# Optimization experiments

Hardware: AMD Instinct MI355X
Metric: run time of the kernel (lower is better)

Reference implementation:

```python
import jax, jax.numpy as jnp
import numpy as np

EPS = 1e-5  # BatchNorm2d default eps
PAD = 7     # width padding; conv-transpose equiv pad = k-1-p = 15-1-7 = 7


def _conv(x, w):
    # NCHW conv, kernel (O,I,1,T), stride 1, padding (0, PAD)
    return jax.lax.conv_general_dilated(
        x, w, window_strides=(1, 1), padding=((0, 0), (PAD, PAD)),
        dimension_numbers=('NCHW', 'OIHW', 'NCHW'))


def setup_inputs() -> dict:
    key = jax.random.key(0)
    ks = jax.random.split(key, 4)
    B, H, D = 32, 64, 256          # batch, electrodes, time (= patch_size = codebook dim)
    C, K, T = 16, 2048, 15         # channel_size, codebook size, temp_kernel
    x = jax.random.normal(ks[0], (B, 1, H, D), dtype=jnp.float32)
    # xavier_uniform_ for both convs (fan_in/fan_out from torch conv weight shapes)
    lim_e = float(np.sqrt(6.0 / (1 * T + C * T)))
    w_enc = jax.random.uniform(ks[1], (C, 1, 1, T), jnp.float32, -lim_e, lim_e)
    lim_d = float(np.sqrt(6.0 / (C * T + 1 * T)))
    # torch ConvTranspose2d weight layout: (in_ch=C, out_ch=1, 1, T)
    w_dec = jax.random.uniform(ks[2], (C, 1, 1, T), jnp.float32, -lim_d, lim_d)
    gamma = jnp.ones((C,), jnp.float32)   # BatchNorm2d weight
    beta = jnp.zeros((C,), jnp.float32)   # BatchNorm2d bias
    emb = jax.random.uniform(ks[3], (K, D), jnp.float32, -1.0 / K, 1.0 / K)
    return dict(x=x, w_enc=w_enc, gamma=gamma, beta=beta, emb=emb, w_dec=w_dec)


def reference(x, w_enc, gamma, beta, emb, w_dec):
    # ---- encode: Conv2d(1,C,(1,T),pad=(0,7),bias=False) + BatchNorm2d (train mode) ----
    z = _conv(x, w_enc)                                   # (B,C,H,D)
    m = z.mean(axis=(0, 2, 3), keepdims=True)
    v = z.var(axis=(0, 2, 3), keepdims=True)
    z_e = gamma[None, :, None, None] * (z - m) * jax.lax.rsqrt(v + EPS) \
        + beta[None, :, None, None]                       # (B,C,H,D)
    # ---- VQ: squared distance to each codeword over the time axis, argmin over K ----
    # dists[b,c,h,k] = sum_d (z_e[b,c,h,d] - emb[k,d])^2, via norm expansion (no (B,K,D,C,H) blowup)
    dots = jnp.einsum('bchd,kd->bchk', z_e, emb)
    dists = (z_e * z_e).sum(-1)[..., None] - 2.0 * dots + (emb * emb).sum(-1)
    latents = jnp.argmin(dists, axis=-1)                  # (B,C,H) int
    # ---- decode: embedding gather + ConvTranspose2d(C,1,(1,T),pad=(0,7)) + tanh ----
    z_q = emb[latents]                                    # (B,C,H,D)
    # stride-1 transposed conv == conv with channel-swapped, spatially-flipped kernel, pad k-1-p
    w_t = jnp.flip(jnp.transpose(w_dec, (1, 0, 2, 3)), axis=(2, 3))  # (1,C,1,T)
    x_tilde = jnp.tanh(_conv(z_q, w_t))                   # (B,1,H,D)
    return x_tilde, z_e, z_q
```

## Files before the change

kernel.cpp:

```cpp
#include <hip/hip_runtime.h>
#include <hip/hip_bf16.h>
#include <cstddef>
#include <cstdint>

#define B   32
#define C   16
#define H   64
#define D   256
#define K   2048
#define T   15
#define PAD 7
#define EPS 1e-5

#define BH      (B*H)
#define ROWS    (B*C*H)
#define N_PER_CH ((double)(B*H*D))
#define NC  8

typedef __attribute__((ext_vector_type(8))) short bf16x8;
typedef __attribute__((ext_vector_type(4))) float f32x4;

__device__ __forceinline__ void gload_lds16(const void* g, void* l) {
  __builtin_amdgcn_global_load_lds(
      (const __attribute__((address_space(1))) unsigned int*)g,
      (__attribute__((address_space(3))) unsigned int*)l, 16, 0, 0);
}

__global__ __launch_bounds__(256) void k0_fused(
    const float* __restrict__ x, const float* __restrict__ w,
    double* __restrict__ partial ,
    const float* __restrict__ emb, double* __restrict__ enorm,
    float* __restrict__ enormf, __hip_bfloat16* __restrict__ embB) {
  __shared__ __attribute__((aligned(16))) float xs[272];
  __shared__ float wsm[C*T];
  const int bh = blockIdx.x, tid = threadIdx.x;
  if (bh >= BH) {
    const int k = (bh - BH) * 4 + (tid >> 6);
    const int lane = tid & 63;
    const float4 ev = *(const float4*)(emb + ((size_t)k << 8) + lane*4);
    __hip_bfloat16 hb[4] = {__float2bfloat16(ev.x), __float2bfloat16(ev.y),
                            __float2bfloat16(ev.z), __float2bfloat16(ev.w)};
    *(int2*)(embB + ((size_t)k << 8) + lane*4) = *(const int2*)hb;
    double s = fma((double)ev.x, (double)ev.x,
               fma((double)ev.y, (double)ev.y,
               fma((double)ev.z, (double)ev.z,
                   (double)ev.w * (double)ev.w)));
#pragma unroll
    for (int off = 1; off < 64; off <<= 1) s += __shfl_xor(s, off, 64);
    if (lane == 0) { enorm[k] = s; enormf[k] = (float)s; }
    return;
  }
  const float* xrow = x + ((size_t)bh << 8);
  if (tid < C*T) wsm[tid] = w[tid];
  xs[tid] = (tid >= 7 && tid < 263) ? xrow[tid - 7] : 0.f;
  if (tid < 16) { int i = 256 + tid; xs[i] = (i < 263) ? xrow[i - 7] : 0.f; }
  __syncthreads();
  const int c = tid >> 4, s = tid & 15;
  float xr[32];
#pragma unroll
  for (int kq = 0; kq < 8; kq++)
    *(float4*)&xr[kq*4] = *(const float4*)&xs[s*16 + kq*4];
  float wv[T];
#pragma unroll
  for (int t = 0; t < T; t++) wv[t] = wsm[c*T + t];
  double sum = 0.0, sq = 0.0;
#pragma unroll
  for (int d0 = 0; d0 < 16; d0++) {
    double z = 0.0;
#pragma unroll
    for (int t = 0; t < T; t++) z = fma((double)wv[t], (double)xr[d0 + t], z);
    sum += z; sq = fma(z, z, sq);
  }
#pragma unroll
  for (int off = 1; off < 16; off <<= 1) {
    sum += __shfl_xor(sum, off, 64);
    sq  += __shfl_xor(sq,  off, 64);
  }
  if (s == 0) {
    partial[((size_t)c*BH + bh)*2 + 0] = sum;
    partial[((size_t)c*BH + bh)*2 + 1] = sq;
  }
}

__global__ __launch_bounds__(256) void k2_stats_final(
    const double* __restrict__ partial, const float* __restrict__ gamma,
    const float* __restrict__ beta, double* __restrict__ params) {
  __shared__ double rs[256], rq[256];
  const int c = blockIdx.x;
  const int tid = threadIdx.x;
  double s = 0.0, q = 0.0;
  for (int i = tid; i < BH; i += 256) {
    s += partial[((size_t)c*BH + i)*2 + 0];
    q += partial[((size_t)c*BH + i)*2 + 1];
  }
  rs[tid] = s; rq[tid] = q;
  __syncthreads();
  for (int off = 128; off; off >>= 1) {
    if (tid < off) { rs[tid] += rs[tid + off]; rq[tid] += rq[tid + off]; }
    __syncthreads();
  }
  if (tid == 0) {
    double m = rs[0] / N_PER_CH;
    double v = rq[0] / N_PER_CH - m * m;
    double a = (double)gamma[c] / sqrt(v + EPS);
    double b = (double)beta[c] - a * m;
    params[c*4+0] = m; params[c*4+1] = v; params[c*4+2] = a; params[c*4+3] = b;
  }
}

__global__ __launch_bounds__(256) void k1b_ze(
    const float* __restrict__ x, const float* __restrict__ w,
    const double* __restrict__ params, float* __restrict__ zE,
    __hip_bfloat16* __restrict__ zEb) {
  __shared__ __attribute__((aligned(16))) float xs[272];
  __shared__ float wsm[C*T];
  const int bh = blockIdx.x, tid = threadIdx.x;
  const int b = bh >> 6, h = bh & 63;
  const float* xrow = x + ((size_t)bh << 8);
  if (tid < C*T) wsm[tid] = w[tid];
  xs[tid] = (tid >= 7 && tid < 263) ? xrow[tid - 7] : 0.f;
  if (tid < 16) { int i = 256 + tid; xs[i] = (i < 263) ? xrow[i - 7] : 0.f; }
  __syncthreads();
  const int c = tid >> 4, s = tid & 15;
  float xr[32];
#pragma unroll
  for (int kq = 0; kq < 8; kq++)
    *(float4*)&xr[kq*4] = *(const float4*)&xs[s*16 + kq*4];
  float wv[T];
#pragma unroll
  for (int t = 0; t < T; t++) wv[t] = wsm[c*T + t];
  const double a = params[c*4+2], bb = params[c*4+3];
  float zf[16];
  __hip_bfloat16 zb[16];
#pragma unroll
  for (int d0 = 0; d0 < 16; d0++) {
    double z = 0.0;
#pragma unroll
    for (int t = 0; t < T; t++) z = fma((double)wv[t], (double)xr[d0 + t], z);
    double ze = fma(a, z, bb);
    zf[d0] = (float)ze;
    zb[d0] = __float2bfloat16(zf[d0]);
  }
  const size_t rbase = ((((size_t)b*C + c)*H + h) << 8) + s*16;
#pragma unroll
  for (int kq = 0; kq < 4; kq++)
    *(float4*)(zE + rbase + kq*4) = *(const float4*)&zf[kq*4];
  *(int4*)(zEb + rbase)     = *(const int4*)&zb[0];
  *(int4*)(zEb + rbase + 8) = *(const int4*)&zb[8];
}

__global__ __launch_bounds__(256, 2) void k4_mfma(
    const __hip_bfloat16* __restrict__ zEb, const __hip_bfloat16* __restrict__ embB,
    const float* __restrict__ enormf, int* __restrict__ cand ) {
  __shared__ __attribute__((aligned(16))) __hip_bfloat16 Ash[64][512];
  __shared__ __attribute__((aligned(16))) __hip_bfloat16 Bsh[2][8][512];

  const int tid  = threadIdx.x;
  const int w    = tid >> 6, lane = tid & 63;
  const int wr   = w >> 1,   wc   = w & 1;
  const int l15  = lane & 15, l4  = lane >> 4;
  const int mblk = blockIdx.x >> 1, nhalf = blockIdx.x & 1;
  const int row0 = mblk * 128;
  const int n0   = nhalf * 1024;

#pragma unroll
  for (int i = 0; i < 16; i++) {
    int f = w*16 + i;
    int kk = f >> 3, mf = f & 7;
    gload_lds16(zEb + (((size_t)(row0 + mf*16 + l15)) << 8) + kk*32 + l4*8,
                &Ash[kk*8 + mf][0]);
  }
  auto stageB = [&](int t) {
    const int slot = t & 1, nt = t >> 3, kk = t & 7;
#pragma unroll
    for (int j = 0; j < 2; j++) {
      int nf = w*2 + j;
      gload_lds16(embB + (((size_t)(n0 + nt*128 + nf*16 + l15)) << 8) + kk*32 + l4*8,
                  &Bsh[slot][nf][0]);
    }
  };
  stageB(0);
  asm volatile("s_waitcnt vmcnt(0) lgkmcnt(0)" ::: "memory");
  __builtin_amdgcn_sched_barrier(0);
  __builtin_amdgcn_s_barrier();

  unsigned t0[16], t1[16];
#pragma unroll
  for (int s = 0; s < 16; s++) { t0[s] = 0xFFFFFFFFu; t1[s] = 0xFFFFFFFFu; }

  f32x4 accA[4][4], accB[4][4];
  float enC0 = 0.f, enC1 = 0.f, enC2 = 0.f, enC3 = 0.f;
  float enP0 = 0.f, enP1 = 0.f, enP2 = 0.f, enP3 = 0.f;

  auto runphase = [&](f32x4 (&ACC)[4][4], f32x4 (&PRV)[4][4],
                      int ntbase, int pnt, bool dp) {
#pragma unroll
    for (int m = 0; m < 4; m++)
#pragma unroll
      for (int n = 0; n < 4; n++) ACC[m][n] = (f32x4){0.f, 0.f, 0.f, 0.f};

#pragma unroll
    for (int kk = 0; kk < 8; kk++) {
      const int t = ntbase*8 + kk;
      if (t) __builtin_amdgcn_s_barrier();
      if (t < 63) {
        stageB(t + 1);
        if (kk == 1) asm volatile("s_waitcnt vmcnt(6)" ::: "memory");
        else         asm volatile("s_waitcnt vmcnt(2)" ::: "memory");
      } else {
        asm volatile("s_waitcnt vmcnt(0)" ::: "memory");
      }
      __builtin_amdgcn_sched_barrier(0);
      __builtin_amdgcn_s_barrier();

      if (kk == 0) {
        enP0 = enC0; enP1 = enC1; enP2 = enC2; enP3 = enC3;
        enC0 = enormf[n0 + ntbase*128 + (wc*4 + 0)*16 + l15];
        enC1 = enormf[n0 + ntbase*128 + (wc*4 + 1)*16 + l15];
        enC2 = enormf[n0 + ntbase*128 + (wc*4 + 2)*16 + l15];
        enC3 = enormf[n0 + ntbase*128 + (wc*4 + 3)*16 + l15];
      }

      bf16x8 af[4], bfr[4];
#pragma unroll
      for (int m = 0; m < 4; m++)
        af[m] = *(const bf16x8*)&Ash[kk*8 + wr*4 + m][lane*8];
#pragma unroll
      for (int n = 0; n < 4; n++)
        bfr[n] = *(const bf16x8*)&Bsh[t & 1][wc*4 + n][lane*8];
#pragma unroll
      for (int m = 0; m < 4; m++)
#pragma unroll
        for (int n = 0; n < 4; n++)
          acc_dummy: ;
#pragma unroll
      for (int m = 0; m < 4; m++)
#pragma unroll
        for (int n = 0; n < 4; n++)
          ACC[m][n] = __builtin_amdgcn_mfma_f32_16x16x32_bf16(af[m], bfr[n], ACC[m][n], 0, 0, 0);

      if (dp) {
        const int n = kk >> 1, hf = kk & 1;
        const float pen = (n == 0) ? enP0 : (n == 1) ? enP1 : (n == 2) ? enP2 : enP3;
        const int pcol = n0 + pnt*128 + (wc*4 + n)*16 + l15;
#pragma unroll
        for (int mm = 0; mm < 2; mm++) {
          const int m = hf*2 + mm;
#pragma unroll
          for (int r = 0; r < 4; r++) {
            const float cv = fmaf(-2.f, PRV[m][n][r], pen);
            unsigned u = __float_as_uint(cv);
            unsigned key = u ^ ((unsigned)((int)u >> 31) | 0x80000000u);
            key = (key & 0xFFFFF800u) | (unsigned)pcol;
            const int s = m*4 + r;
            unsigned mx = key > t0[s] ? key : t0[s];
            t0[s] = key < t0[s] ? key : t0[s];
            t1[s] = mx < t1[s] ? mx : t1[s];
          }
        }
      }
    }
  };

  for (int nt = 0; nt < 8; nt += 2) {
    runphase(accA, accB, nt,     nt - 1, nt > 0);
    runphase(accB, accA, nt + 1, nt,     true);
  }
#pragma unroll
  for (int kk = 0; kk < 8; kk++) {
    const int n = kk >> 1, hf = kk & 1;
    const float pen = (n == 0) ? enC0 : (n == 1) ? enC1 : (n == 2) ? enC2 : enC3;
    const int pcol = n0 + 7*128 + (wc*4 + n)*16 + l15;
#pragma unroll
    for (int mm = 0; mm < 2; mm++) {
      const int m = hf*2 + mm;
#pragma unroll
      for (int r = 0; r < 4; r++) {
        const float cv = fmaf(-2.f, accB[m][n][r], pen);
        unsigned u = __float_as_uint(cv);
        unsigned key = u ^ ((unsigned)((int)u >> 31) | 0x80000000u);
        key = (key & 0xFFFFF800u) | (unsigned)pcol;
        const int s = m*4 + r;
        unsigned mx = key > t0[s] ? key : t0[s];
        t0[s] = key < t0[s] ? key : t0[s];
        t1[s] = mx < t1[s] ? mx : t1[s];
      }
    }
  }

  __syncthreads();
  unsigned* KeyM = (unsigned*)&Ash[0][0];
  const int tk = wc*16 + l15;
#pragma unroll
  for (int s = 0; s < 16; s++) {
    const int r = wr*64 + (s >> 2)*16 + l4*4 + (s & 3);
    KeyM[r*65 + tk*2 + 0] = t0[s];
    KeyM[r*65 + tk*2 + 1] = t1[s];
  }
  __syncthreads();
  if (tid < 128) {
    unsigned bk[4];
#pragma unroll
    for (int j = 0; j < 4; j++) bk[j] = 0xFFFFFFFFu;
    for (int e = 0; e < 64; e++) {
      unsigned v = KeyM[tid*65 + e];
      if (v < bk[3]) {
        int j = 3;
        while (j > 0 && v < bk[j-1]) { bk[j] = bk[j-1]; j--; }
        bk[j] = v;
      }
    }
    int* cr = cand + ((size_t)(row0 + tid)) * NC + nhalf*4;
#pragma unroll
    for (int j = 0; j < 4; j++) cr[j] = (int)(bk[j] & 2047u);
  }
}

__global__ __launch_bounds__(256) void k5_fused(
    const float* __restrict__ zE, const float* __restrict__ emb,
    const double* __restrict__ enorm, const int* __restrict__ cand,
    const float* __restrict__ wdec,
    float* __restrict__ zq, float* __restrict__ xt) {
  __shared__ __attribute__((aligned(16))) float zsh[C][256];
  __shared__ __attribute__((aligned(16))) float zs[C][272];
  __shared__ __attribute__((aligned(16))) float part[4][256];
  __shared__ float wt[C*T];
  __shared__ int bkS[C];
  const int bh = blockIdx.x, b = bh >> 6, h = bh & 63;
  const int tid = threadIdx.x;
  const int wv = tid >> 6, lane = tid & 63;

#pragma unroll
  for (int i = 0; i < 4; i++) {
    int p = i*256 + tid;
    int c = p >> 6, cc = p & 63;
    gload_lds16(zE + ((((size_t)b*C + c)*H + h) << 8) + cc*4, &zsh[c][cc*4]);
  }
  if (tid < C*T) { int c = tid / T, t = tid % T; wt[c*T + t] = wdec[c*T + (T-1-t)]; }
  asm volatile("s_waitcnt vmcnt(0)" ::: "memory");
  __syncthreads();

  const int j = lane >> 3, q = lane & 7;
#pragma unroll
  for (int i = 0; i < 4; i++) {
    const int c = wv*4 + i;
    const size_t rid = ((size_t)b*C + c)*H + h;
    const int k = cand[rid * NC + j];
    const float* er = emb + ((size_t)k << 8);
    double a0 = 0.0, a1 = 0.0, a2 = 0.0, a3 = 0.0;
#pragma unroll
    for (int it = 0; it < 8; it++) {
      const int e0 = it*32 + q*4;
      const float4 ev = *(const float4*)(er + e0);
      const float4 zv = *(const float4*)&zsh[c][e0];
      a0 = fma((double)ev.x, (double)zv.x, a0);
      a1 = fma((double)ev.y, (double)zv.y, a1);
      a2 = fma((double)ev.z, (double)zv.z, a2);
      a3 = fma((double)ev.w, (double)zv.w, a3);
    }
    double dot = (a0 + a1) + (a2 + a3);
    dot += __shfl_xor(dot, 1, 64);
    dot += __shfl_xor(dot, 2, 64);
    dot += __shfl_xor(dot, 4, 64);
    double cv = enorm[k] - 2.0 * dot;
    int bk = k;
#pragma unroll
    for (int off = 8; off < 64; off <<= 1) {
      double ocv = __shfl_xor(cv, off, 64);
      int    okk = __shfl_xor(bk, off, 64);
      if (ocv < cv || (ocv == cv && okk < bk)) { cv = ocv; bk = okk; }
    }
    if (lane == 0) bkS[c] = bk;
  }
  __syncthreads();

  for (int i2 = tid; i2 < C*D; i2 += 256) {
    int c = i2 >> 8, dd = i2 & 255;
    float v = emb[((size_t)bkS[c] << 8) + dd];
    zs[c][dd + PAD] = v;
    zq[((((size_t)b*C + c)*H + h) << 8) + dd] = v;
  }
  { int jj = tid & 15, c = tid >> 4;
    int pos = (jj < 7) ? jj : (256 + PAD + (jj - 7));
    zs[c][pos] = 0.f; }
  __syncthreads();

  const int dg = tid & 63, cg = tid >> 6;
  float f[20];
  float oo[4] = {0.f, 0.f, 0.f, 0.f};
#pragma unroll
  for (int ci = 0; ci < 4; ci++) {
    const int c = cg*4 + ci;
#pragma unroll
    for (int kq = 0; kq < 5; kq++)
      *(float4*)&f[kq*4] = *(const float4*)&zs[c][dg*4 + kq*4];
#pragma unroll
    for (int jj = 0; jj < 4; jj++)
#pragma unroll
      for (int t = 0; t < T; t++)
        oo[jj] = fmaf(wt[c*T + t], f[jj + t], oo[jj]);
  }
  *(float4*)&part[cg][dg*4] = make_float4(oo[0], oo[1], oo[2], oo[3]);
  __syncthreads();
  float r = part[0][tid] + part[1][tid] + part[2][tid] + part[3][tid];
  xt[((size_t)bh << 8) + tid] = tanhf(r);
}

extern "C" void kernel_launch(void* const* d_in, const int* in_sizes, int n_in,
                              void* d_out, int out_size, void* d_ws, size_t ws_size,
                              hipStream_t stream) {
  const float* x     = (const float*)d_in[0];
  const float* w_enc = (const float*)d_in[1];
  const float* gamma = (const float*)d_in[2];
  const float* beta  = (const float*)d_in[3];
  const float* emb   = (const float*)d_in[4];
  const float* w_dec = (const float*)d_in[5];

  float* out = (float*)d_out;
  float* xt = out;
  float* zE = out + (size_t)B*H*D;
  float* zq = out + (size_t)B*H*D + (size_t)B*C*H*D;

  char* ws = (char*)d_ws;
  double* partial = (double*)(ws);
  double* params  = (double*)(ws + 524288);
  double* enorm   = (double*)(ws + 524800);
  float*  enormf  = (float*) (ws + 541184);
  int*    cand    = (int*)   (ws + 549376);
  __hip_bfloat16* zEb  = (__hip_bfloat16*)(ws + 1597952);
  __hip_bfloat16* embB = (__hip_bfloat16*)(ws + 18375168);

  k0_fused<<<BH + 512, 256, 0, stream>>>(x, w_enc, partial, emb, enorm, enormf, embB);
  k2_stats_final<<<C, 256, 0, stream>>>(partial, gamma, beta, params);
  k1b_ze<<<BH, 256, 0, stream>>>(x, w_enc, params, zE, zEb);
  k4_mfma<<<512, 256, 0, stream>>>(zEb, embB, enormf, cand);
  k5_fused<<<BH, 256, 0, stream>>>(zE, emb, enorm, cand, w_dec, zq, xt);
}
```

Baseline: 145.9 us.

## Move exact fp64 candidate rescoring into the MFMA kernel, slim decode kernel

The fp64 rescoring of the top-4 bf16 candidates per half now runs at the end of the MFMA kernel, which writes one best value and index per row-half. The decode kernel only merges the two halves and skips reloading z_e into LDS. This removes the candidate-list round trip and the heavy rescoring stage from the decode kernel. In exchange, each thread in the MFMA epilogue does a serial 256-element fp64 dot product from global memory, which may be slow and uncoalesced.

Measured after the change: 147.3 us. No clear change (+1.0%).

```diff
diff --git a/kernel.cpp b/kernel.cpp
--- a/kernel.cpp
+++ b/kernel.cpp
@@ -15,7 +15,6 @@
 #define BH      (B*H)
 #define ROWS    (B*C*H)
 #define N_PER_CH ((double)(B*H*D))
-#define NC  8
 
 typedef __attribute__((ext_vector_type(8))) short bf16x8;
 typedef __attribute__((ext_vector_type(4))) float f32x4;
@@ -151,7 +150,9 @@
 
 __global__ __launch_bounds__(256, 2) void k4_mfma(
     const __hip_bfloat16* __restrict__ zEb, const __hip_bfloat16* __restrict__ embB,
-    const float* __restrict__ enormf, int* __restrict__ cand ) {
+    const float* __restrict__ enormf, const float* __restrict__ zE,
+    const float* __restrict__ emb, const double* __restrict__ enorm,
+    double* __restrict__ rscV, int* __restrict__ rscK) {
   __shared__ __attribute__((aligned(16))) __hip_bfloat16 Ash[64][512];
   __shared__ __attribute__((aligned(16))) __hip_bfloat16 Bsh[2][8][512];
 
@@ -232,11 +233,6 @@
       for (int m = 0; m < 4; m++)
 #pragma unroll
         for (int n = 0; n < 4; n++)
-          acc_dummy: ;
-#pragma unroll
-      for (int m = 0; m < 4; m++)
-#pragma unroll
-        for (int n = 0; n < 4; n++)
           ACC[m][n] = __builtin_amdgcn_mfma_f32_16x16x32_bf16(af[m], bfr[n], ACC[m][n], 0, 0, 0);
 
       if (dp) {
@@ -290,6 +286,8 @@
 
   __syncthreads();
   unsigned* KeyM = (unsigned*)&Ash[0][0];
+  int*    candS = (int*)&Bsh[0][0][0];
+  double* cvS   = (double*)(candS + 512);
   const int tk = wc*16 + l15;
 #pragma unroll
   for (int s = 0; s < 16; s++) {
@@ -310,67 +308,75 @@
         bk[j] = v;
       }
     }
-    int* cr = cand + ((size_t)(row0 + tid)) * NC + nhalf*4;
-#pragma unroll
-    for (int j = 0; j < 4; j++) cr[j] = (int)(bk[j] & 2047u);
-  }
-}
-
-__global__ __launch_bounds__(256) void k5_fused(
-    const float* __restrict__ zE, const float* __restrict__ emb,
-    const double* __restrict__ enorm, const int* __restrict__ cand,
-    const float* __restrict__ wdec,
+#pragma unroll
+    for (int j = 0; j < 4; j++) candS[tid*4 + j] = (int)(bk[j] & 2047u);
+  }
+  __syncthreads();
+
+#pragma unroll
+  for (int i = 0; i < 2; i++) {
+    const int task = tid + 256*i;
+    const int r = task >> 2, cj = task & 3;
+    const int k = candS[r*4 + cj];
+    const float* zr = zE + ((size_t)(row0 + r) << 8);
+    const float* er = emb + ((size_t)k << 8);
+    double a0 = 0.0, a1 = 0.0, a2 = 0.0, a3 = 0.0;
+    for (int it = 0; it < 16; it++) {
+      const int e0 = it*16;
+      const float4 z0 = *(const float4*)(zr + e0);
+      const float4 e0v = *(const float4*)(er + e0);
+      const float4 z1 = *(const float4*)(zr + e0 + 4);
+      const float4 e1v = *(const float4*)(er + e0 + 4);
+      const float4 z2 = *(const float4*)(zr + e0 + 8);
+      const float4 e2v = *(const float4*)(er + e0 + 8);
+      const float4 z3 = *(const float4*)(zr + e0 + 12);
+      const float4 e3v = *(const float4*)(er + e0 + 12);
+      a0 = fma((double)e0v.x, (double)z0.x, fma((double)e0v.y, (double)z0.y,
+           fma((double)e0v.z, (double)z0.z, fma((double)e0v.w, (double)z0.w, a0))));
+      a1 = fma((double)e1v.x, (double)z1.x, fma((double)e1v.y, (double)z1.y,
+           fma((double)e1v.z, (double)z1.z, fma((double)e1v.w, (double)z1.w, a1))));
+      a2 = fma((double)e2v.x, (double)z2.x, fma((double)e2v.y, (double)z2.y,
+           fma((double)e2v.z, (double)z2.z, fma((double)e2v.w, (double)z2.w, a2))));
+      a3 = fma((double)e3v.x, (double)z3.x, fma((double)e3v.y, (double)z3.y,
+           fma((double)e3v.z, (double)z3.z, fma((double)e3v.w, (double)z3.w, a3))));
+    }
+    const double dot = (a0 + a1) + (a2 + a3);
+    cvS[r*4 + cj] = enorm[k] - 2.0 * dot;
+  }
+  __syncthreads();
+  if (tid < 128) {
+    double bv = cvS[tid*4 + 0]; int bk = candS[tid*4 + 0];
+#pragma unroll
+    for (int j = 1; j < 4; j++) {
+      double v = cvS[tid*4 + j]; int kj = candS[tid*4 + j];
+      if (v < bv || (v == bv && kj < bk)) { bv = v; bk = kj; }
+    }
+    const size_t rid = (size_t)(row0 + tid);
+    rscV[rid*2 + nhalf] = bv;
+    rscK[rid*2 + nhalf] = bk;
+  }
+}
+
+__global__ __launch_bounds__(256) void k7_decode(
+    const float* __restrict__ emb, const double* __restrict__ rscV,
+    const int* __restrict__ rscK, const float* __restrict__ wdec,
     float* __restrict__ zq, float* __restrict__ xt) {
-  __shared__ __attribute__((aligned(16))) float zsh[C][256];
   __shared__ __attribute__((aligned(16))) float zs[C][272];
   __shared__ __attribute__((aligned(16))) float part[4][256];
   __shared__ float wt[C*T];
   __shared__ int bkS[C];
   const int bh = blockIdx.x, b = bh >> 6, h = bh & 63;
   const int tid = threadIdx.x;
-  const int wv = tid >> 6, lane = tid & 63;
-
-#pragma unroll
-  for (int i = 0; i < 4; i++) {
-    int p = i*256 + tid;
-    int c = p >> 6, cc = p & 63;
-    gload_lds16(zE + ((((size_t)b*C + c)*H + h) << 8) + cc*4, &zsh[c][cc*4]);
-  }
-  if (tid < C*T) { int c = tid / T, t = tid % T; wt[c*T + t] = wdec[c*T + (T-1-t)]; }
-  asm volatile("s_waitcnt vmcnt(0)" ::: "memory");
-  __syncthreads();
-
-  const int j = lane >> 3, q = lane & 7;
-#pragma unroll
-  for (int i = 0; i < 4; i++) {
-    const int c = wv*4 + i;
-    const size_t rid = ((size_t)b*C + c)*H + h;
-    const int k = cand[rid * NC + j];
-    const float* er = emb + ((size_t)k << 8);
-    double a0 = 0.0, a1 = 0.0, a2 = 0.0, a3 = 0.0;
-#pragma unroll
-    for (int it = 0; it < 8; it++) {
-      const int e0 = it*32 + q*4;
-      const float4 ev = *(const float4*)(er + e0);
-      const float4 zv = *(const float4*)&zsh[c][e0];
-      a0 = fma((double)ev.x, (double)zv.x, a0);
-      a1 = fma((double)ev.y, (double)zv.y, a1);
-      a2 = fma((double)ev.z, (double)zv.z, a2);
-      a3 = fma((double)ev.w, (double)zv.w, a3);
-    }
-    double dot = (a0 + a1) + (a2 + a3);
-    dot += __shfl_xor(dot, 1, 64);
-    dot += __shfl_xor(dot, 2, 64);
-    dot += __shfl_xor(dot, 4, 64);
-    double cv = enorm[k] - 2.0 * dot;
-    int bk = k;
-#pragma unroll
-    for (int off = 8; off < 64; off <<= 1) {
-      double ocv = __shfl_xor(cv, off, 64);
-      int    okk = __shfl_xor(bk, off, 64);
-      if (ocv < cv || (ocv == cv && okk < bk)) { cv = ocv; bk = okk; }
-    }
-    if (lane == 0) bkS[c] = bk;
+
+  if (tid < C) {
+    const size_t rid = ((size_t)b*C + tid)*H + h;
+    const double cv0 = rscV[rid*2 + 0], cv1 = rscV[rid*2 + 1];
+    const int    k0  = rscK[rid*2 + 0], k1  = rscK[rid*2 + 1];
+    bkS[tid] = (cv1 < cv0 || (cv1 == cv0 && k1 < k0)) ? k1 : k0;
+  }
+  if (tid < C*T) {
+    int c = tid / T, t = tid % T;
+    wt[c*T + t] = wdec[c*T + (T-1-t)];
   }
   __syncthreads();
 
@@ -426,13 +432,14 @@
   double* params  = (double*)(ws + 524288);
   double* enorm   = (double*)(ws + 524800);
   float*  enormf  = (float*) (ws + 541184);
-  int*    cand    = (int*)   (ws + 549376);
-  __hip_bfloat16* zEb  = (__hip_bfloat16*)(ws + 1597952);
-  __hip_bfloat16* embB = (__hip_bfloat16*)(ws + 18375168);
+  double* rscV    = (double*)(ws + 549376);
+  int*    rscK    = (int*)   (ws + 1073664);
+  __hip_bfloat16* zEb  = (__hip_bfloat16*)(ws + 1335808);
+  __hip_bfloat16* embB = (__hip_bfloat16*)(ws + 18113024);
 
   k0_fused<<<BH + 512, 256, 0, stream>>>(x, w_enc, partial, emb, enorm, enormf, embB);
   k2_stats_final<<<C, 256, 0, stream>>>(partial, gamma, beta, params);
   k1b_ze<<<BH, 256, 0, stream>>>(x, w_enc, params, zE, zEb);
-  k4_mfma<<<512, 256, 0, stream>>>(zEb, embB, enormf, cand);
-  k5_fused<<<BH, 256, 0, stream>>>(zE, emb, enorm, cand, w_dec, zq, xt);
-}
+  k4_mfma<<<512, 256, 0, stream>>>(zEb, embB, enormf, zE, emb, enorm, rscV, rscK);
+  k7_decode<<<BH, 256, 0, stream>>>(emb, rscV, rscK, w_dec, zq, xt);
+}
```

## Split fp64 candidate rescoring out of decode kernel into separate per-row kernel

Applied to the files above, without the earlier changes.

Moves the fp64 rescoring of the top-8 candidate codewords out of the fused decode kernel into its own kernel. In that kernel each wavefront handles one row, and two half-waves each reduce four candidates and write their winners to workspace. The decode kernel then picks between the two winners and does the gather and transposed conv. The aim is more parallelism and simpler blocks for the rescore phase, at the cost of an extra launch and a small workspace round-trip. It also removes a dead empty loop in the MFMA kernel.

After: 131.2 us, median of 3. 1.11x faster.

```diff
diff --git a/kernel.cpp b/kernel.cpp
--- a/kernel.cpp
+++ b/kernel.cpp
@@ -232,11 +232,6 @@
       for (int m = 0; m < 4; m++)
 #pragma unroll
         for (int n = 0; n < 4; n++)
-          acc_dummy: ;
-#pragma unroll
-      for (int m = 0; m < 4; m++)
-#pragma unroll
-        for (int n = 0; n < 4; n++)
           ACC[m][n] = __builtin_amdgcn_mfma_f32_16x16x32_bf16(af[m], bfr[n], ACC[m][n], 0, 0, 0);
 
       if (dp) {
@@ -316,61 +311,65 @@
   }
 }
 
-__global__ __launch_bounds__(256) void k5_fused(
+__global__ __launch_bounds__(256) void k6_rescore(
     const float* __restrict__ zE, const float* __restrict__ emb,
     const double* __restrict__ enorm, const int* __restrict__ cand,
-    const float* __restrict__ wdec,
+    double* __restrict__ rscV, int* __restrict__ rscK) {
+  const int wv = threadIdx.x >> 6, lane = threadIdx.x & 63;
+  const size_t row = (size_t)blockIdx.x * 4 + wv;
+  const int j = lane >> 3, q = lane & 7;
+  const int k = cand[row * NC + j];
+  const float* er = emb + ((size_t)k << 8);
+  const float* zr = zE + (row << 8);
+  double a0 = 0.0, a1 = 0.0, a2 = 0.0, a3 = 0.0;
+#pragma unroll
+  for (int it = 0; it < 8; it++) {
+    const int e0 = it*32 + q*4;
+    const float4 ev = *(const float4*)(er + e0);
+    const float4 zv = *(const float4*)(zr + e0);
+    a0 = fma((double)ev.x, (double)zv.x, a0);
+    a1 = fma((double)ev.y, (double)zv.y, a1);
+    a2 = fma((double)ev.z, (double)zv.z, a2);
+    a3 = fma((double)ev.w, (double)zv.w, a3);
+  }
+  double dot = (a0 + a1) + (a2 + a3);
+  dot += __shfl_xor(dot, 1, 64);
+  dot += __shfl_xor(dot, 2, 64);
+  dot += __shfl_xor(dot, 4, 64);
+  double cv = enorm[k] - 2.0 * dot;
+  int bk = k;
+#pragma unroll
+  for (int off = 8; off < 32; off <<= 1) {
+    double ocv = __shfl_xor(cv, off, 64);
+    int    okk = __shfl_xor(bk, off, 64);
+    if (ocv < cv || (ocv == cv && okk < bk)) { cv = ocv; bk = okk; }
+  }
+  if ((lane & 31) == 0) {
+    rscV[row*2 + (lane >> 5)] = cv;
+    rscK[row*2 + (lane >> 5)] = bk;
+  }
+}
+
+__global__ __launch_bounds__(256) void k7_decode(
+    const float* __restrict__ emb, const double* __restrict__ rscV,
+    const int* __restrict__ rscK, const float* __restrict__ wdec,
     float* __restrict__ zq, float* __restrict__ xt) {
-  __shared__ __attribute__((aligned(16))) float zsh[C][256];
   __shared__ __attribute__((aligned(16))) float zs[C][272];
   __shared__ __attribute__((aligned(16))) float part[4][256];
   __shared__ float wt[C*T];
   __shared__ int bkS[C];
   const int bh = blockIdx.x, b = bh >> 6, h = bh & 63;
   const int tid = threadIdx.x;
-  const int wv = tid >> 6, lane = tid & 63;
-
-#pragma unroll
-  for (int i = 0; i < 4; i++) {
-    int p = i*256 + tid;
-    int c = p >> 6, cc = p & 63;
-    gload_lds16(zE + ((((size_t)b*C + c)*H + h) << 8) + cc*4, &zsh[c][cc*4]);
-  }
-  if (tid < C*T) { int c = tid / T, t = tid % T; wt[c*T + t] = wdec[c*T + (T-1-t)]; }
-  asm volatile("s_waitcnt vmcnt(0)" ::: "memory");
-  __syncthreads();
-
-  const int j = lane >> 3, q = lane & 7;
-#pragma unroll
-  for (int i = 0; i < 4; i++) {
-    const int c = wv*4 + i;
-    const size_t rid = ((size_t)b*C + c)*H + h;
-    const int k = cand[rid * NC + j];
-    const float* er = emb + ((size_t)k << 8);
-    double a0 = 0.0, a1 = 0.0, a2 = 0.0, a3 = 0.0;
-#pragma unroll
-    for (int it = 0; it < 8; it++) {
-      const int e0 = it*32 + q*4;
-      const float4 ev = *(const float4*)(er + e0);
-      const float4 zv = *(const float4*)&zsh[c][e0];
-      a0 = fma((double)ev.x, (double)zv.x, a0);
-      a1 = fma((double)ev.y, (double)zv.y, a1);
-      a2 = fma((double)ev.z, (double)zv.z, a2);
-      a3 = fma((double)ev.w, (double)zv.w, a3);
-    }
-    double dot = (a0 + a1) + (a2 + a3);
-    dot += __shfl_xor(dot, 1, 64);
-    dot += __shfl_xor(dot, 2, 64);
-    dot += __shfl_xor(dot, 4, 64);
-    double cv = enorm[k] - 2.0 * dot;
-    int bk = k;
-#pragma unroll
-    for (int off = 8; off < 64; off <<= 1) {
-      double ocv = __shfl_xor(cv, off, 64);
-      int    okk = __shfl_xor(bk, off, 64);
-      if (ocv < cv || (ocv == cv && okk < bk)) { cv = ocv; bk = okk; }
-    }
-    if (lane == 0) bkS[c] = bk;
+
+  if (tid < C) {
+    const size_t rid = ((size_t)b*C + tid)*H + h;
+    const double cv0 = rscV[rid*2 + 0], cv1 = rscV[rid*2 + 1];
+    const int    k0  = rscK[rid*2 + 0], k1  = rscK[rid*2 + 1];
+    bkS[tid] = (cv1 < cv0 || (cv1 == cv0 && k1 < k0)) ? k1 : k0;
+  }
+  if (tid < C*T) {
+    int c = tid / T, t = tid % T;
+    wt[c*T + t] = wdec[c*T + (T-1-t)];
   }
   __syncthreads();
 
@@ -427,12 +426,15 @@
   double* enorm   = (double*)(ws + 524800);
   float*  enormf  = (float*) (ws + 541184);
   int*    cand    = (int*)   (ws + 549376);
-  __hip_bfloat16* zEb  = (__hip_bfloat16*)(ws + 1597952);
-  __hip_bfloat16* embB = (__hip_bfloat16*)(ws + 18375168);
+  double* rscV    = (double*)(ws + 1597952);
+  int*    rscK    = (int*)   (ws + 2122240);
+  __hip_bfloat16* zEb  = (__hip_bfloat16*)(ws + 2384384);
+  __hip_bfloat16* embB = (__hip_bfloat16*)(ws + 19161600);
 
   k0_fused<<<BH + 512, 256, 0, stream>>>(x, w_enc, partial, emb, enorm, enormf, embB);
   k2_stats_final<<<C, 256, 0, stream>>>(partial, gamma, beta, params);
   k1b_ze<<<BH, 256, 0, stream>>>(x, w_enc, params, zE, zEb);
   k4_mfma<<<512, 256, 0, stream>>>(zEb, embB, enormf, cand);
-  k5_fused<<<BH, 256, 0, stream>>>(zE, emb, enorm, cand, w_dec, zq, xt);
-}
+  k6_rescore<<<ROWS/4, 256, 0, stream>>>(zE, emb, enorm, cand, rscV, rscK);
+  k7_decode<<<BH, 256, 0, stream>>>(emb, rscV, rscK, w_dec, zq, xt);
+}
```
